# Performance work log

Hardware: AMD Instinct MI355X
Metric: run time of the kernel (lower is better)

Reference implementation:

```python
import jax, jax.numpy as jnp
import numpy as np

INPUT_SIZE = 100
HIDDEN_SIZE = 200
OUTPUT_SIZE = 1


def setup_inputs() -> dict:
    key = jax.random.key(0)
    k0, k1, k2, k3, k4, k5, k6 = jax.random.split(key, 7)
    s = 1.0 / np.sqrt(HIDDEN_SIZE)  # torch RNNCell/Linear init scale
    inp = jax.random.normal(k0, (128, 1024, INPUT_SIZE), dtype=jnp.float32)
    W_ih = jax.random.uniform(k1, (HIDDEN_SIZE, INPUT_SIZE), minval=-s, maxval=s)
    W_hh = jax.random.uniform(k2, (HIDDEN_SIZE, HIDDEN_SIZE), minval=-s, maxval=s)
    b_ih = jax.random.uniform(k3, (HIDDEN_SIZE,), minval=-s, maxval=s)
    b_hh = jax.random.uniform(k4, (HIDDEN_SIZE,), minval=-s, maxval=s)
    W_out = jax.random.uniform(k5, (OUTPUT_SIZE, HIDDEN_SIZE), minval=-s, maxval=s)
    b_out = jax.random.uniform(k6, (OUTPUT_SIZE,), minval=-s, maxval=s)
    return {"input": inp, "W_ih": W_ih, "W_hh": W_hh, "b_ih": b_ih,
            "b_hh": b_hh, "W_out": W_out, "b_out": b_out}


def reference(input, W_ih, W_hh, b_ih, b_hh, W_out, b_out):
    B, T, _ = input.shape
    # Precompute input projections for all timesteps in one GEMM: [B,T,H]
    x_proj = jnp.einsum('bti,hi->bth', input, W_ih) + b_ih + b_hh

    def step(h, xp_t):  # h: [B,H], xp_t: [B,H]
        h = jax.nn.relu(xp_t + h @ W_hh.T)
        o = h @ W_out.T + b_out  # identity output nonlinearity (out_nlin='linear')
        return h, (h, o)

    h0 = jnp.zeros((B, HIDDEN_SIZE), dtype=input.dtype)
    _, (hiddens, outputs) = jax.lax.scan(step, h0, jnp.swapaxes(x_proj, 0, 1))
    outputs = jnp.swapaxes(outputs, 0, 1)  # [B,T,O]
    hiddens = jnp.swapaxes(hiddens, 0, 1)  # [B,T,H] (torch returns list of [B,H])
    return (outputs, hiddens)
```

## Files before the change

kernel.cpp:

```cpp
#include <hip/hip_runtime.h>

#define BB 128
#define TT 1024
#define II 100
#define HH 200

#define PIN4(v) asm volatile("" : "+v"((v).x), "+v"((v).y), "+v"((v).z), "+v"((v).w))

__global__ __launch_bounds__(256, 1) void rnn_xproj(
    const float* __restrict__ x, const float* __restrict__ Wih,
    const float* __restrict__ bih, const float* __restrict__ bhh,
    float* __restrict__ hid)
{
    __shared__ __align__(16) float xs[128 * II];
    const int tid = threadIdx.x;
    const int j = tid;
    const int jl = (j < HH) ? j : (HH - 1);

    float4 w[25];
    const float4* wrow = (const float4*)(Wih + jl * II);
#pragma unroll
    for (int kk = 0; kk < 25; ++kk) { w[kk] = wrow[kk]; PIN4(w[kk]); }
    const float bias = bih[jl] + bhh[jl];

    const long long r0 = (long long)blockIdx.x * 128;
    const float4* src = (const float4*)(x + r0 * II);
    float4* dst = (float4*)xs;
    for (int p = tid; p < 128 * II / 4; p += 256) dst[p] = src[p];
    __syncthreads();

    for (int row = 0; row < 128; ++row) {
        float a0 = 0.f, a1 = 0.f, a2 = 0.f, a3 = 0.f;
        const float4* xr = (const float4*)(xs + row * II);
#pragma unroll
        for (int kk = 0; kk < 25; ++kk) {
            float4 v = xr[kk];
            a0 += w[kk].x * v.x; a1 += w[kk].y * v.y;
            a2 += w[kk].z * v.z; a3 += w[kk].w * v.w;
        }
        if (j < HH)
            hid[(r0 + row) * HH + j] = bias + ((a0 + a1) + (a2 + a3));
    }
}

__global__ __launch_bounds__(512, 2) void rnn_recur(
    const float* __restrict__ Whh, float* __restrict__ hid)
{
    __shared__ __align__(16) float hbuf[2][208];
    const int tid  = threadIdx.x;
    const int half = tid & 1;
    const int j    = tid >> 1;
    const bool act = (j < HH);
    const int  jl  = act ? j : (HH - 1);

    float4 w[25];
    const float4* wrow = (const float4*)(Whh + jl * HH + 100 * half);
#pragma unroll
    for (int kk = 0; kk < 25; ++kk) { w[kk] = wrow[kk]; PIN4(w[kk]); }

    if (tid < HH) hbuf[0][tid] = 0.f;
    __syncthreads();

    float* rowp = hid + (long long)blockIdx.x * TT * HH;
    float xpv = (act && half == 0) ? rowp[j] : 0.f;
    int cur = 0;

    for (int t = 0; t < TT; ++t) {
        float xpn = 0.f;
        if (act && half == 0 && t + 1 < TT) xpn = rowp[HH + j];

        const float4* hr = (const float4*)(hbuf[cur] + 100 * half);
        float a0 = 0.f, a1 = 0.f, a2 = 0.f, a3 = 0.f;
#pragma unroll
        for (int kk = 0; kk < 25; ++kk) {
            float4 v = hr[kk];
            a0 += w[kk].x * v.x; a1 += w[kk].y * v.y;
            a2 += w[kk].z * v.z; a3 += w[kk].w * v.w;
        }
        float p = (a0 + a1) + (a2 + a3);
        p += __shfl_xor(p, 1, 64);

        if (act && half == 0) {
            float hv = fmaxf(xpv + p, 0.f);
            rowp[j] = hv;
            hbuf[cur ^ 1][j] = hv;
        }
        __syncthreads();
        cur ^= 1; xpv = xpn; rowp += HH;
    }
}

__global__ __launch_bounds__(256) void rnn_out(
    const float* __restrict__ hid, const float* __restrict__ Wout,
    const float* __restrict__ bout, float* __restrict__ out)
{
    const int wave = threadIdx.x >> 6;
    const int lane = threadIdx.x & 63;

    float wv[4];
#pragma unroll
    for (int m = 0; m < 4; ++m) {
        int idx = lane + 64 * m;
        wv[m] = (idx < HH) ? Wout[idx] : 0.f;
    }
    const float bo = bout[0];

    const long long rbase = (long long)blockIdx.x * 64;
#pragma unroll 1
    for (int rr = wave; rr < 64; rr += 4) {
        const float* hr = hid + (rbase + rr) * HH;
        float p = 0.f;
#pragma unroll
        for (int m = 0; m < 4; ++m) {
            int idx = lane + 64 * m;
            if (idx < HH) p += wv[m] * hr[idx];
        }
#pragma unroll
        for (int off = 32; off; off >>= 1) p += __shfl_down(p, off, 64);
        if (lane == 0) out[rbase + rr] = p + bo;
    }
}

extern "C" void kernel_launch(void* const* d_in, const int* in_sizes, int n_in,
                              void* d_out, int out_size, void* d_ws, size_t ws_size,
                              hipStream_t stream)
{
    const float* x    = (const float*)d_in[0];
    const float* Wih  = (const float*)d_in[1];
    const float* Whh  = (const float*)d_in[2];
    const float* bih  = (const float*)d_in[3];
    const float* bhh  = (const float*)d_in[4];
    const float* Wout = (const float*)d_in[5];
    const float* bout = (const float*)d_in[6];

    float* out = (float*)d_out;
    float* hid = out + (long long)BB * TT;

    rnn_xproj<<<(BB * TT) / 128, 256, 0, stream>>>(x, Wih, bih, bhh, hid);
    rnn_recur<<<BB, 512, 0, stream>>>(Whh, hid);
    rnn_out<<<(BB * TT) / 64, 256, 0, stream>>>(hid, Wout, bout, out);
}
```

Baseline: 1.187 ms.

## Split recurrent matvec 4-way across waves with readlane broadcast of hidden state

The recurrent kernel now uses 1024 threads per batch row. Each output unit's dot product is split into four 50-element quarters handled by separate waves. Each lane loads one hidden value from LDS and the wave broadcasts it with readlane, instead of every thread reading float4 from shared memory. Partial sums are combined through a small LDS buffer, at the cost of a second barrier per timestep and many scalar readlane ops. The register pinning in the input-projection kernel is also dropped.

New measurement: 1.244 ms. +4.9%, slower.

```diff
diff --git a/kernel.cpp b/kernel.cpp
--- a/kernel.cpp
+++ b/kernel.cpp
@@ -4,8 +4,6 @@
 #define TT 1024
 #define II 100
 #define HH 200
-
-#define PIN4(v) asm volatile("" : "+v"((v).x), "+v"((v).y), "+v"((v).z), "+v"((v).w))
 
 __global__ __launch_bounds__(256, 1) void rnn_xproj(
     const float* __restrict__ x, const float* __restrict__ Wih,
@@ -20,7 +18,7 @@
     float4 w[25];
     const float4* wrow = (const float4*)(Wih + jl * II);
 #pragma unroll
-    for (int kk = 0; kk < 25; ++kk) { w[kk] = wrow[kk]; PIN4(w[kk]); }
+    for (int kk = 0; kk < 25; ++kk) w[kk] = wrow[kk];
     const float bias = bih[jl] + bhh[jl];
 
     const long long r0 = (long long)blockIdx.x * 128;
@@ -43,50 +41,68 @@
     }
 }
 
-__global__ __launch_bounds__(512, 2) void rnn_recur(
+__global__ __launch_bounds__(1024, 1) void rnn_recur(
     const float* __restrict__ Whh, float* __restrict__ hid)
 {
-    __shared__ __align__(16) float hbuf[2][208];
+    __shared__ float hbuf[256];
+    __shared__ float pbuf[3][256];
+
     const int tid  = threadIdx.x;
-    const int half = tid & 1;
-    const int j    = tid >> 1;
-    const bool act = (j < HH);
-    const int  jl  = act ? j : (HH - 1);
+    const int wv   = tid >> 6;
+    const int lane = tid & 63;
+    const int jgrp = wv & 3;
+    const int q    = wv >> 2;
+    const int j2   = jgrp * 64 + lane;
+    const bool jact = (j2 < HH);
+    const int  jl   = jact ? j2 : (HH - 1);
 
-    float4 w[25];
-    const float4* wrow = (const float4*)(Whh + jl * HH + 100 * half);
+    float w[50];
+    {
+        const float2* wp = (const float2*)(Whh + jl * HH + 50 * q);
 #pragma unroll
-    for (int kk = 0; kk < 25; ++kk) { w[kk] = wrow[kk]; PIN4(w[kk]); }
+        for (int kk = 0; kk < 25; ++kk) {
+            float2 v = wp[kk];
+            w[2 * kk] = v.x; w[2 * kk + 1] = v.y;
+        }
+#pragma unroll
+        for (int kk = 0; kk < 50; ++kk) asm volatile("" : "+v"(w[kk]));
+    }
 
-    if (tid < HH) hbuf[0][tid] = 0.f;
+    if (tid < 256) hbuf[tid] = 0.f;
     __syncthreads();
 
     float* rowp = hid + (long long)blockIdx.x * TT * HH;
-    float xpv = (act && half == 0) ? rowp[j] : 0.f;
-    int cur = 0;
+    float xpv = (q == 0 && jact) ? rowp[j2] : 0.f;
 
+#pragma unroll 1
     for (int t = 0; t < TT; ++t) {
+        float hA = hbuf[50 * q + lane];
+
         float xpn = 0.f;
-        if (act && half == 0 && t + 1 < TT) xpn = rowp[HH + j];
+        if (q == 0 && jact && t + 1 < TT) xpn = rowp[HH + j2];
 
-        const float4* hr = (const float4*)(hbuf[cur] + 100 * half);
         float a0 = 0.f, a1 = 0.f, a2 = 0.f, a3 = 0.f;
 #pragma unroll
-        for (int kk = 0; kk < 25; ++kk) {
-            float4 v = hr[kk];
-            a0 += w[kk].x * v.x; a1 += w[kk].y * v.y;
-            a2 += w[kk].z * v.z; a3 += w[kk].w * v.w;
+        for (int kk = 0; kk < 48; kk += 4) {
+            a0 += w[kk + 0] * __int_as_float(__builtin_amdgcn_readlane(__float_as_int(hA), kk + 0));
+            a1 += w[kk + 1] * __int_as_float(__builtin_amdgcn_readlane(__float_as_int(hA), kk + 1));
+            a2 += w[kk + 2] * __int_as_float(__builtin_amdgcn_readlane(__float_as_int(hA), kk + 2));
+            a3 += w[kk + 3] * __int_as_float(__builtin_amdgcn_readlane(__float_as_int(hA), kk + 3));
         }
+        a0 += w[48] * __int_as_float(__builtin_amdgcn_readlane(__float_as_int(hA), 48));
+        a1 += w[49] * __int_as_float(__builtin_amdgcn_readlane(__float_as_int(hA), 49));
         float p = (a0 + a1) + (a2 + a3);
-        p += __shfl_xor(p, 1, 64);
 
-        if (act && half == 0) {
-            float hv = fmaxf(xpv + p, 0.f);
-            rowp[j] = hv;
-            hbuf[cur ^ 1][j] = hv;
+        if (q > 0) pbuf[q - 1][j2] = p;
+        __syncthreads();
+
+        if (q == 0) {
+            float s = p + pbuf[0][j2] + pbuf[1][j2] + pbuf[2][j2];
+            float hv = fmaxf(xpv + s, 0.f);
+            if (jact) { rowp[j2] = hv; hbuf[j2] = hv; }
         }
         __syncthreads();
-        cur ^= 1; xpv = xpn; rowp += HH;
+        xpv = xpn; rowp += HH;
     }
 }
 
@@ -137,6 +153,6 @@
     float* hid = out + (long long)BB * TT;
 
     rnn_xproj<<<(BB * TT) / 128, 256, 0, stream>>>(x, Wih, bih, bhh, hid);
-    rnn_recur<<<BB, 512, 0, stream>>>(Whh, hid);
+    rnn_recur<<<BB, 1024, 0, stream>>>(Whh, hid);
     rnn_out<<<(BB * TT) / 64, 256, 0, stream>>>(hid, Wout, bout, out);
 }
```

## Batch 16 sequences per block and run recurrence on fp16 MFMA

Applied to the files above, without the earlier changes.

The recurrent kernel now handles 16 batch rows per block and computes h @ W_hh^T with 16x16x32 fp16 MFMA instructions. W_hh is held in registers as fp16 fragments, and the hidden state is kept in LDS as fp16. This replaces one block per sequence doing scalar FP32 dot products, so each weight load is reused across 16 sequences and matrix cores do the work. In exchange only 8 blocks run, far fewer than the CUs available, and rounding h and W_hh to fp16 every step can let error build up over 1024 steps.

After: 1.181 ms. Within noise of the previous version (-0.5%).

```diff
diff --git a/kernel.cpp b/kernel.cpp
--- a/kernel.cpp
+++ b/kernel.cpp
@@ -4,8 +4,14 @@
 #define TT 1024
 #define II 100
 #define HH 200
-
-#define PIN4(v) asm volatile("" : "+v"((v).x), "+v"((v).y), "+v"((v).z), "+v"((v).w))
+#define MB 16
+#define NTL 13
+#define KST 7
+#define HSTR 232
+
+typedef _Float16 half8  __attribute__((ext_vector_type(8)));
+typedef _Float16 half4v __attribute__((ext_vector_type(4)));
+typedef float    f32x4  __attribute__((ext_vector_type(4)));
 
 __global__ __launch_bounds__(256, 1) void rnn_xproj(
     const float* __restrict__ x, const float* __restrict__ Wih,
@@ -20,7 +26,7 @@
     float4 w[25];
     const float4* wrow = (const float4*)(Wih + jl * II);
 #pragma unroll
-    for (int kk = 0; kk < 25; ++kk) { w[kk] = wrow[kk]; PIN4(w[kk]); }
+    for (int kk = 0; kk < 25; ++kk) w[kk] = wrow[kk];
     const float bias = bih[jl] + bhh[jl];
 
     const long long r0 = (long long)blockIdx.x * 128;
@@ -43,50 +49,109 @@
     }
 }
 
-__global__ __launch_bounds__(512, 2) void rnn_recur(
-    const float* __restrict__ Whh, float* __restrict__ hid)
-{
-    __shared__ __align__(16) float hbuf[2][208];
-    const int tid  = threadIdx.x;
-    const int half = tid & 1;
-    const int j    = tid >> 1;
-    const bool act = (j < HH);
-    const int  jl  = act ? j : (HH - 1);
-
-    float4 w[25];
-    const float4* wrow = (const float4*)(Whh + jl * HH + 100 * half);
-#pragma unroll
-    for (int kk = 0; kk < 25; ++kk) { w[kk] = wrow[kk]; PIN4(w[kk]); }
-
-    if (tid < HH) hbuf[0][tid] = 0.f;
+__global__ __launch_bounds__(256, 1) __attribute__((amdgpu_waves_per_eu(1, 1)))
+void rnn_recur(const float* __restrict__ Whh, float* __restrict__ hid)
+{
+    __shared__ _Float16 hl[2][MB][HSTR];
+
+    const int tid = threadIdx.x;
+    const int wv  = tid >> 6;
+    const int l   = tid & 63;
+    const int m   = l & 15;
+    const int kq  = l >> 4;
+
+    half8 wf[4][KST];
+#pragma unroll
+    for (int i = 0; i < 4; ++i) {
+        const int nt = 4 * i + wv;
+        const bool v = (nt < NTL);
+        int j = 16 * nt + m; if (j > HH - 1) j = HH - 1;
+#pragma unroll
+        for (int ks = 0; ks < KST; ++ks) {
+            const int k0 = 32 * ks + 8 * kq;
+            half8 f;
+#pragma unroll
+            for (int e = 0; e < 8; ++e) f[e] = (_Float16)0.f;
+            if (v && k0 < HH) {
+                const float4 lo = *(const float4*)(Whh + j * HH + k0);
+                const float4 hi = *(const float4*)(Whh + j * HH + k0 + 4);
+                f[0] = (_Float16)lo.x; f[1] = (_Float16)lo.y;
+                f[2] = (_Float16)lo.z; f[3] = (_Float16)lo.w;
+                f[4] = (_Float16)hi.x; f[5] = (_Float16)hi.y;
+                f[6] = (_Float16)hi.z; f[7] = (_Float16)hi.w;
+            }
+            wf[i][ks] = f;
+        }
+    }
+
+    int  j0a[4]; bool stv[4];
+#pragma unroll
+    for (int i = 0; i < 4; ++i) {
+        const int nt = 4 * i + wv;
+        j0a[i] = 16 * nt + 4 * kq;
+        stv[i] = (nt < NTL) && (j0a[i] < HH);
+    }
+
+    {
+        int* zp = (int*)hl;
+        for (int p = tid; p < (int)(sizeof(hl) / 4); p += 256) zp[p] = 0;
+    }
     __syncthreads();
 
-    float* rowp = hid + (long long)blockIdx.x * TT * HH;
-    float xpv = (act && half == 0) ? rowp[j] : 0.f;
+    const long long TTHH = (long long)TT * HH;
+    float* mybase = hid + (long long)blockIdx.x * MB * TTHH + (long long)m * TTHH;
+
+    float4 xpv[4];
+#pragma unroll
+    for (int i = 0; i < 4; ++i)
+        xpv[i] = stv[i] ? *(const float4*)(mybase + j0a[i])
+                        : make_float4(0.f, 0.f, 0.f, 0.f);
+
     int cur = 0;
-
+#pragma unroll 1
     for (int t = 0; t < TT; ++t) {
-        float xpn = 0.f;
-        if (act && half == 0 && t + 1 < TT) xpn = rowp[HH + j];
-
-        const float4* hr = (const float4*)(hbuf[cur] + 100 * half);
-        float a0 = 0.f, a1 = 0.f, a2 = 0.f, a3 = 0.f;
-#pragma unroll
-        for (int kk = 0; kk < 25; ++kk) {
-            float4 v = hr[kk];
-            a0 += w[kk].x * v.x; a1 += w[kk].y * v.y;
-            a2 += w[kk].z * v.z; a3 += w[kk].w * v.w;
-        }
-        float p = (a0 + a1) + (a2 + a3);
-        p += __shfl_xor(p, 1, 64);
-
-        if (act && half == 0) {
-            float hv = fmaxf(xpv + p, 0.f);
-            rowp[j] = hv;
-            hbuf[cur ^ 1][j] = hv;
-        }
+        float4 xpn[4];
+        const bool pf = (t + 1 < TT);
+#pragma unroll
+        for (int i = 0; i < 4; ++i)
+            xpn[i] = (pf && stv[i])
+                   ? *(const float4*)(mybase + (long long)(t + 1) * HH + j0a[i])
+                   : make_float4(0.f, 0.f, 0.f, 0.f);
+
+        half8 bf[KST];
+        const _Float16* hb = &hl[cur][m][0];
+#pragma unroll
+        for (int ks = 0; ks < KST; ++ks)
+            bf[ks] = *(const half8*)(hb + 32 * ks + 8 * kq);
+
+        f32x4 acc[4];
+#pragma unroll
+        for (int i = 0; i < 4; ++i) acc[i] = (f32x4){0.f, 0.f, 0.f, 0.f};
+#pragma unroll
+        for (int ks = 0; ks < KST; ++ks) {
+#pragma unroll
+            for (int i = 0; i < 4; ++i)
+                acc[i] = __builtin_amdgcn_mfma_f32_16x16x32_f16(
+                    wf[i][ks], bf[ks], acc[i], 0, 0, 0);
+        }
+
+#pragma unroll
+        for (int i = 0; i < 4; ++i) {
+            if (!stv[i]) continue;
+            const float h0 = fmaxf(acc[i][0] + xpv[i].x, 0.f);
+            const float h1 = fmaxf(acc[i][1] + xpv[i].y, 0.f);
+            const float h2 = fmaxf(acc[i][2] + xpv[i].z, 0.f);
+            const float h3 = fmaxf(acc[i][3] + xpv[i].w, 0.f);
+            *(float4*)(mybase + (long long)t * HH + j0a[i]) =
+                make_float4(h0, h1, h2, h3);
+            half4v pk = {(_Float16)h0, (_Float16)h1, (_Float16)h2, (_Float16)h3};
+            *(half4v*)&hl[cur ^ 1][m][j0a[i]] = pk;
+        }
+
         __syncthreads();
-        cur ^= 1; xpv = xpn; rowp += HH;
+        cur ^= 1;
+#pragma unroll
+        for (int i = 0; i < 4; ++i) xpv[i] = xpn[i];
     }
 }
 
@@ -99,9 +164,9 @@
 
     float wv[4];
 #pragma unroll
-    for (int m = 0; m < 4; ++m) {
-        int idx = lane + 64 * m;
-        wv[m] = (idx < HH) ? Wout[idx] : 0.f;
+    for (int mi = 0; mi < 4; ++mi) {
+        int idx = lane + 64 * mi;
+        wv[mi] = (idx < HH) ? Wout[idx] : 0.f;
     }
     const float bo = bout[0];
 
@@ -111,9 +176,9 @@
         const float* hr = hid + (rbase + rr) * HH;
         float p = 0.f;
 #pragma unroll
-        for (int m = 0; m < 4; ++m) {
-            int idx = lane + 64 * m;
-            if (idx < HH) p += wv[m] * hr[idx];
+        for (int mi = 0; mi < 4; ++mi) {
+            int idx = lane + 64 * mi;
+            if (idx < HH) p += wv[mi] * hr[idx];
         }
 #pragma unroll
         for (int off = 32; off; off >>= 1) p += __shfl_down(p, off, 64);
@@ -137,6 +202,6 @@
     float* hid = out + (long long)BB * TT;
 
     rnn_xproj<<<(BB * TT) / 128, 256, 0, stream>>>(x, Wih, bih, bhh, hid);
-    rnn_recur<<<BB, 512, 0, stream>>>(Whh, hid);
+    rnn_recur<<<BB / MB, 256, 0, stream>>>(Whh, hid);
     rnn_out<<<(BB * TT) / 64, 256, 0, stream>>>(hid, Wout, bout, out);
 }
```
